# Performance work log

Hardware: AMD Instinct MI355X
Metric: run time of the kernel (lower is better)

## Reference

```python
import jax, jax.numpy as jnp
import numpy as np

N = 50000
E = 800000
IN_DIM = 3
HID = 128
OUT_DIM = 3
RED = 16


def setup_inputs() -> dict:
    key = jax.random.key(0)
    ks = jax.random.split(key, 20)
    s = lambda k, shp: jax.random.normal(k, shp, dtype=jnp.float32) * 0.05
    inp = {
        'x': jax.random.normal(ks[0], (N, IN_DIM), dtype=jnp.float32),
        'edge_index': jax.random.randint(ks[1], (2, E), 0, N, dtype=jnp.int32),
        'deg_inv_sqrt': jax.random.uniform(ks[2], (N,), dtype=jnp.float32),
        # GCN layer weights (torch Linear convention: [out, in])
        'W1': s(ks[3], (HID, IN_DIM)), 'b1': s(ks[4], (HID,)),
        'W2': s(ks[5], (HID, HID)),    'b2': s(ks[6], (HID,)),
        'W3': s(ks[7], (HID, HID)),    'b3': s(ks[8], (HID,)),
        # channel attention MLPs (no bias): C -> C//RED -> C
        'ca1_w1': s(ks[9],  (HID // RED, HID)), 'ca1_w2': s(ks[10], (HID, HID // RED)),
        'ca2_w1': s(ks[11], (HID // RED, HID)), 'ca2_w2': s(ks[12], (HID, HID // RED)),
        'ca3_w1': s(ks[13], (HID // RED, HID)), 'ca3_w2': s(ks[14], (HID, HID // RED)),
        # output head
        'Wout': s(ks[15], (OUT_DIM, HID)), 'bout': s(ks[16], (OUT_DIM,)),
    }
    return inp


def _gcn(x, row, col, dis, W, b):
    # gather source features, normalize by deg_inv_sqrt[row]*deg_inv_sqrt[col], scatter-add to target
    norm = (dis[row] * dis[col])[:, None]          # [E,1]
    msg = x[row] * norm                             # [E,C]
    agg = jax.ops.segment_sum(msg, col, num_segments=x.shape[0])  # [N,C]
    return jax.nn.elu(agg @ W.T + b)


def _channel_attn(x, w1, w2):
    # global avg/max pool over nodes -> [C]; shared MLP; sigmoid gate
    avg = jnp.mean(x, axis=0)
    mx = jnp.max(x, axis=0)
    mlp = lambda v: jax.nn.relu(v @ w1.T) @ w2.T
    att = jax.nn.sigmoid(mlp(avg) + mlp(mx))        # [C]
    return x * att


def reference(x, edge_index, deg_inv_sqrt, W1, b1, W2, b2, W3, b3,
              ca1_w1, ca1_w2, ca2_w1, ca2_w2, ca3_w1, ca3_w2, Wout, bout):
    row, col = edge_index[0], edge_index[1]
    h = _gcn(x, row, col, deg_inv_sqrt, W1, b1)
    h = _channel_attn(h, ca1_w1, ca1_w2)
    h = _gcn(h, row, col, deg_inv_sqrt, W2, b2)
    h = _channel_attn(h, ca2_w1, ca2_w2)
    h = _gcn(h, row, col, deg_inv_sqrt, W3, b3)
    h = _channel_attn(h, ca3_w1, ca3_w2)
    return h @ Wout.T + bout
```

## Files before the change

kernel.cpp:

```cpp
#include <hip/hip_runtime.h>

#define NN 50000
#define NE 800000
#define NPAD 50176
#define NBD3 391
#define NBG 782
#define PMAX (NBG*128)
#define NRED 64

#define EC 4096
#define NBLKC 196
#define NBUCK 1563
#define LT (NBUCK*NBLKC)
#define NS1 300
#define DCAP 1024

typedef __attribute__((ext_vector_type(8))) short bf16x8;
typedef __attribute__((ext_vector_type(4))) float f32x4;

__device__ __forceinline__ float elu_f(float x){ return x > 0.f ? x : __expf(x) - 1.f; }

__device__ __forceinline__ ushort f2bf(float f){
    unsigned u = __float_as_uint(f);
    unsigned r = (u + 0x7FFFu + ((u >> 16) & 1u)) >> 16;
    return (ushort)r;
}
__device__ __forceinline__ float bf2f(short u){
    return __uint_as_float(((unsigned)(unsigned short)u) << 16);
}

__global__ __launch_bounds__(256) void k_bhist(const int* __restrict__ col, int* __restrict__ hist,
                        const float* __restrict__ W2, const float* __restrict__ W3,
                        ushort* __restrict__ Wb2, ushort* __restrict__ Wb3){
    int blk = blockIdx.x;
    if (blk >= NBLKC){
        int i = (blk - NBLKC)*256 + threadIdx.x;
        if (i < 16384){ Wb2[i] = f2bf(W2[i]); Wb3[i] = f2bf(W3[i]); }
        return;
    }
    __shared__ int h[NBUCK];
    for (int i = threadIdx.x; i < NBUCK; i += 256) h[i] = 0;
    __syncthreads();
    int base = blk * EC;
    #pragma unroll
    for (int i = 0; i < 16; ++i){
        int e = base + i*256 + threadIdx.x;
        if (e < NE) atomicAdd(&h[col[e] >> 5], 1);
    }
    __syncthreads();
    for (int i = threadIdx.x; i < NBUCK; i += 256) hist[i*NBLKC + blk] = h[i];
}

__global__ __launch_bounds__(256) void k_s1(const int* __restrict__ hist, int* __restrict__ bsum){
    __shared__ int red[256];
    int base = blockIdx.x*1024 + threadIdx.x;
    int s = 0;
    #pragma unroll
    for (int i = 0; i < 4; ++i){ int idx = base + i*256; if (idx < LT) s += hist[idx]; }
    red[threadIdx.x] = s;
    __syncthreads();
    for (int off = 128; off > 0; off >>= 1){
        if (threadIdx.x < off) red[threadIdx.x] += red[threadIdx.x + off];
        __syncthreads();
    }
    if (threadIdx.x == 0) bsum[blockIdx.x] = red[0];
}

__global__ __launch_bounds__(512) void k_s2(const int* __restrict__ bsum, int* __restrict__ boff){
    __shared__ int s[512];
    int t = threadIdx.x;
    int v = (t < NS1) ? bsum[t] : 0;
    s[t] = v;
    __syncthreads();
    for (int off = 1; off < 512; off <<= 1){
        int u = (t >= off) ? s[t - off] : 0;
        __syncthreads();
        s[t] += u;
        __syncthreads();
    }
    if (t < NS1) boff[t] = s[t] - v;
}

__global__ __launch_bounds__(256) void k_s3(const int* __restrict__ hist, const int* __restrict__ boff,
                                            int* __restrict__ scanned, int* __restrict__ bucketPtr){
    __shared__ int red[256];
    int blk = blockIdx.x, t = threadIdx.x;
    int base = blk*1024;
    int v[4]; int s = 0;
    #pragma unroll
    for (int i = 0; i < 4; ++i){
        int idx = base + t*4 + i;
        v[i] = (idx < LT) ? hist[idx] : 0;
        s += v[i];
    }
    red[t] = s;
    __syncthreads();
    for (int off = 1; off < 256; off <<= 1){
        int u = (t >= off) ? red[t - off] : 0;
        __syncthreads();
        red[t] += u;
        __syncthreads();
    }
    int run = boff[blk] + red[t] - s;
    #pragma unroll
    for (int i = 0; i < 4; ++i){
        int idx = base + t*4 + i;
        if (idx < LT){
            scanned[idx] = run;
            if (idx % NBLKC == 0) bucketPtr[idx / NBLKC] = run;
            run += v[i];
        }
    }
    if (blk == 0 && t == 0) bucketPtr[NBUCK] = NE;
}

__global__ __launch_bounds__(256) void k_csort(const int* __restrict__ row, const int* __restrict__ col,
                                               const int* __restrict__ scanned, int2* __restrict__ edgeS){
    __shared__ int curs[NBUCK];
    int blk = blockIdx.x;
    for (int i = threadIdx.x; i < NBUCK; i += 256) curs[i] = scanned[i*NBLKC + blk];
    __syncthreads();
    int base = blk * EC;
    #pragma unroll
    for (int i = 0; i < 16; ++i){
        int e = base + i*256 + threadIdx.x;
        if (e < NE){
            int r = row[e], c = col[e];
            int pos = atomicAdd(&curs[c >> 5], 1);
            edgeS[pos] = make_int2(r, c);
        }
    }
}

__global__ __launch_bounds__(256) void k_dsort(const float* __restrict__ dis, const int* __restrict__ bucketPtr,
                                               int2* __restrict__ edge, int* __restrict__ rowptr){
    __shared__ int nodeCnt[32];
    __shared__ int nodeOff[33];
    __shared__ float disL[32];
    __shared__ int2 stage[DCAP];
    int b = blockIdx.x, t = threadIdx.x;
    int j0 = bucketPtr[b], j1 = bucketPtr[b+1], cnt = j1 - j0;
    if (t < 32){
        nodeCnt[t] = 0;
        int c = b*32 + t;
        disL[t] = (c < NN) ? dis[c] : 0.f;
    }
    __syncthreads();
    int er[8], ec[8], rk[8]; int m = 0;
    for (int j = t; j < cnt && m < 8; j += 256){
        int2 e = edge[j0 + j];
        int cl = e.y & 31;
        er[m] = e.x; ec[m] = e.y;
        rk[m] = atomicAdd(&nodeCnt[cl], 1);
        ++m;
    }
    __syncthreads();
    if (t == 0){
        int run = 0;
        #pragma unroll
        for (int i = 0; i < 32; ++i){ nodeOff[i] = run; run += nodeCnt[i]; }
        nodeOff[32] = run;
    }
    __syncthreads();
    if (t < 32){
        int c = b*32 + t;
        if (c < NN) rowptr[c] = j0 + nodeOff[t];
    }
    if (b == 0 && t == 0) rowptr[NN] = NE;
    bool staged = (cnt <= DCAP);
    for (int i = 0; i < m; ++i){
        int r = er[i], cl = ec[i] & 31;
        float nm = dis[r] * disL[cl];
        int pos = nodeOff[cl] + rk[i];
        int2 rec = make_int2(r, __float_as_int(nm));
        if (staged) stage[pos] = rec;
        else        edge[j0 + pos] = rec;
    }
    __syncthreads();
    if (staged)
        for (int j = t; j < cnt; j += 256) edge[j0 + j] = stage[j];
}

__global__ void k_gather3(const float* __restrict__ x, const int* __restrict__ rowptr,
                          const int2* __restrict__ edge, float* __restrict__ agg){
    int n = blockIdx.x * blockDim.x + threadIdx.x;
    if (n >= NN) return;
    int j0 = rowptr[n], j1 = rowptr[n + 1];
    float a0 = 0.f, a1 = 0.f, a2 = 0.f;
    for (int j = j0; j < j1; ++j){
        int2 e = edge[j];
        int r = e.x; float w = __int_as_float(e.y);
        a0 = fmaf(x[r*3+0], w, a0);
        a1 = fmaf(x[r*3+1], w, a1);
        a2 = fmaf(x[r*3+2], w, a2);
    }
    agg[n*3+0] = a0; agg[n*3+1] = a1; agg[n*3+2] = a2;
}

__global__ __launch_bounds__(128) void k_dense3p(const float* __restrict__ agg, const float* __restrict__ W,
                          const float* __restrict__ b, ushort* __restrict__ h, float* __restrict__ part){
    int c = threadIdx.x;
    int n0 = blockIdx.x * 128;
    int n1 = min(n0 + 128, NN);
    float w0 = W[c*3+0], w1 = W[c*3+1], w2 = W[c*3+2], bb = b[c];
    float s = 0.f, m = -3.4e38f;
    for (int n = n0; n < n1; ++n){
        float v = fmaf(agg[n*3+0], w0, fmaf(agg[n*3+1], w1, fmaf(agg[n*3+2], w2, bb)));
        v = elu_f(v);
        h[(size_t)n*128 + c] = f2bf(v);
        s += v; m = fmaxf(m, v);
    }
    part[blockIdx.x*128 + c] = s;
    part[PMAX + blockIdx.x*128 + c] = m;
}

__global__ __launch_bounds__(256) void k_gather128(const ushort* __restrict__ h,
                              const int* __restrict__ rowptr, const int2* __restrict__ edge,
                              const float* __restrict__ att, ushort* __restrict__ aggB){
    int t = blockIdx.x * blockDim.x + threadIdx.x;
    int n = t >> 4, l = t & 15;
    if (n >= NN) return;
    int j0 = rowptr[n], j1 = rowptr[n + 1];
    float acc[8] = {0.f,0.f,0.f,0.f,0.f,0.f,0.f,0.f};
    int j = j0;
    for (; j + 3 < j1; j += 4){
        int2 e0 = edge[j], e1 = edge[j+1], e2 = edge[j+2], e3 = edge[j+3];
        bf16x8 v0 = *(const bf16x8*)(h + (size_t)e0.x*128 + l*8);
        bf16x8 v1 = *(const bf16x8*)(h + (size_t)e1.x*128 + l*8);
        bf16x8 v2 = *(const bf16x8*)(h + (size_t)e2.x*128 + l*8);
        bf16x8 v3 = *(const bf16x8*)(h + (size_t)e3.x*128 + l*8);
        float w0 = __int_as_float(e0.y), w1 = __int_as_float(e1.y);
        float w2 = __int_as_float(e2.y), w3 = __int_as_float(e3.y);
        #pragma unroll
        for (int c = 0; c < 8; ++c){
            acc[c] = fmaf(bf2f(v0[c]), w0, acc[c]);
            acc[c] = fmaf(bf2f(v1[c]), w1, acc[c]);
            acc[c] = fmaf(bf2f(v2[c]), w2, acc[c]);
            acc[c] = fmaf(bf2f(v3[c]), w3, acc[c]);
        }
    }
    for (; j < j1; ++j){
        int2 e0 = edge[j];
        bf16x8 v0 = *(const bf16x8*)(h + (size_t)e0.x*128 + l*8);
        float w0 = __int_as_float(e0.y);
        #pragma unroll
        for (int c = 0; c < 8; ++c)
            acc[c] = fmaf(bf2f(v0[c]), w0, acc[c]);
    }
    float4 a0 = ((const float4*)att)[l*2];
    float4 a1 = ((const float4*)att)[l*2+1];
    float av[8] = {a0.x,a0.y,a0.z,a0.w,a1.x,a1.y,a1.z,a1.w};
    bf16x8 o;
    #pragma unroll
    for (int c = 0; c < 8; ++c)
        o[c] = (short)f2bf(acc[c] * av[c]);
    *(bf16x8*)(aggB + (size_t)n*128 + l*8) = o;
}

__global__ __launch_bounds__(256) void k_attn_pre(const float* __restrict__ part, int nblk,
                                                  float* __restrict__ part2){
    __shared__ float sS[2][128], sM[2][128];
    int c = threadIdx.x & 127, g = threadIdx.x >> 7;
    float s = 0.f, m = -3.4e38f;
    for (int b = blockIdx.x*2 + g; b < nblk; b += NRED*2){
        s += part[b*128 + c];
        m = fmaxf(m, part[PMAX + b*128 + c]);
    }
    sS[g][c] = s; sM[g][c] = m;
    __syncthreads();
    if (g == 0){
        part2[blockIdx.x*128 + c] = sS[0][c] + sS[1][c];
        part2[NRED*128 + blockIdx.x*128 + c] = fmaxf(sM[0][c], sM[1][c]);
    }
}

__global__ __launch_bounds__(512) void k_attn(const float* __restrict__ part2,
                       const float* __restrict__ w1, const float* __restrict__ w2,
                       float* __restrict__ att){
    __shared__ float sAll[4][128], mAll[4][128];
    __shared__ float avg[128], mx[128], ha[8], hm[8];
    int c = threadIdx.x & 127, g = threadIdx.x >> 7;
    float s = 0.f, m = -3.4e38f;
    #pragma unroll
    for (int b = 0; b < NRED/4; ++b){
        int r = b*4 + g;
        s += part2[r*128 + c];
        m = fmaxf(m, part2[NRED*128 + r*128 + c]);
    }
    sAll[g][c] = s; mAll[g][c] = m;
    __syncthreads();
    if (g == 0){
        s = sAll[0][c] + sAll[1][c] + sAll[2][c] + sAll[3][c];
        m = fmaxf(fmaxf(mAll[0][c], mAll[1][c]), fmaxf(mAll[2][c], mAll[3][c]));
        avg[c] = s / (float)NN;
        mx[c] = m;
    }
    __syncthreads();
    if (threadIdx.x < 8){
        int cc = threadIdx.x;
        float sa = 0.f, sm = 0.f;
        for (int k = 0; k < 128; ++k){
            float w = w1[cc*128 + k];
            sa += avg[k]*w; sm += mx[k]*w;
        }
        ha[cc] = fmaxf(sa, 0.f); hm[cc] = fmaxf(sm, 0.f);
    }
    __syncthreads();
    if (threadIdx.x < 128){
        float oa = 0.f, om = 0.f;
        for (int j = 0; j < 8; ++j){
            float w = w2[c*8 + j];
            oa += ha[j]*w; om += hm[j]*w;
        }
        att[c] = 1.f / (1.f + __expf(-(oa + om)));
    }
}

__global__ __launch_bounds__(256) void k_gemm_mfma(const ushort* __restrict__ aggB,
                        const ushort* __restrict__ Wb, const float* __restrict__ b,
                        ushort* __restrict__ h, float* __restrict__ part){
    __shared__ float poolS[4][128], poolM[4][128];
    int tid = threadIdx.x;
    int wave = tid >> 6, l = tid & 63;
    int lr = l & 15, lk = l >> 4;
    int n0 = blockIdx.x * 64 + wave * 16;

    bf16x8 a[4];
    const ushort* arow = aggB + (size_t)(n0 + lr) * 128 + lk * 8;
    #pragma unroll
    for (int kb = 0; kb < 4; ++kb)
        a[kb] = *(const bf16x8*)(arow + kb * 32);

    float s_part[8], m_part[8];
    const ushort* wbase = Wb + (size_t)lr * 128 + lk * 8;
    #pragma unroll
    for (int t = 0; t < 8; ++t){
        int j0 = t * 16;
        float bias = b[j0 + lr];
        f32x4 acc = {bias, bias, bias, bias};
        const ushort* wrow = wbase + (size_t)j0 * 128;
        #pragma unroll
        for (int kb = 0; kb < 4; ++kb){
            bf16x8 bf = *(const bf16x8*)(wrow + kb * 32);
            acc = __builtin_amdgcn_mfma_f32_16x16x32_bf16(a[kb], bf, acc, 0, 0, 0);
        }
        float s = 0.f, m = -3.4e38f;
        #pragma unroll
        for (int r = 0; r < 4; ++r){
            int n = n0 + lk * 4 + r;
            float v = elu_f(acc[r]);
            if (n < NN){
                h[(size_t)n * 128 + j0 + lr] = f2bf(v);
                s += v; m = fmaxf(m, v);
            }
        }
        s += __shfl_xor(s, 16); s += __shfl_xor(s, 32);
        m = fmaxf(m, __shfl_xor(m, 16)); m = fmaxf(m, __shfl_xor(m, 32));
        s_part[t] = s; m_part[t] = m;
    }
    if (lk == 0){
        #pragma unroll
        for (int t = 0; t < 8; ++t){
            poolS[wave][t * 16 + lr] = s_part[t];
            poolM[wave][t * 16 + lr] = m_part[t];
        }
    }
    __syncthreads();
    if (tid < 128){
        float S = poolS[0][tid] + poolS[1][tid] + poolS[2][tid] + poolS[3][tid];
        float M = fmaxf(fmaxf(poolM[0][tid], poolM[1][tid]), fmaxf(poolM[2][tid], poolM[3][tid]));
        part[blockIdx.x * 128 + tid] = S;
        part[PMAX + blockIdx.x * 128 + tid] = M;
    }
}

__global__ __launch_bounds__(256) void k_out(const ushort* __restrict__ h, const float* __restrict__ att,
                      const float* __restrict__ Wo, const float* __restrict__ bo,
                      float* __restrict__ out){
    int n = blockIdx.x * blockDim.x + threadIdx.x;
    if (n >= NN) return;
    float acc0 = bo[0], acc1 = bo[1], acc2 = bo[2];
    const bf16x8* hv = (const bf16x8*)(h + (size_t)n*128);
    #pragma unroll
    for (int i = 0; i < 16; ++i){
        bf16x8 v = hv[i];
        #pragma unroll
        for (int c = 0; c < 8; ++c){
            int cc = i*8 + c;
            float hv_f = bf2f(v[c]) * att[cc];
            acc0 = fmaf(hv_f, Wo[cc],        acc0);
            acc1 = fmaf(hv_f, Wo[128 + cc],  acc1);
            acc2 = fmaf(hv_f, Wo[256 + cc],  acc2);
        }
    }
    out[n*3+0] = acc0; out[n*3+1] = acc1; out[n*3+2] = acc2;
}

extern "C" void kernel_launch(void* const* d_in, const int* in_sizes, int n_in,
                              void* d_out, int out_size, void* d_ws, size_t ws_size,
                              hipStream_t stream) {
    const float* x    = (const float*)d_in[0];
    const int*   ei   = (const int*)d_in[1];
    const int*   row  = ei;
    const int*   col  = ei + NE;
    const float* dis  = (const float*)d_in[2];
    const float* W1   = (const float*)d_in[3];
    const float* b1   = (const float*)d_in[4];
    const float* W2   = (const float*)d_in[5];
    const float* b2   = (const float*)d_in[6];
    const float* W3   = (const float*)d_in[7];
    const float* b3   = (const float*)d_in[8];
    const float* ca1w1= (const float*)d_in[9];
    const float* ca1w2= (const float*)d_in[10];
    const float* ca2w1= (const float*)d_in[11];
    const float* ca2w2= (const float*)d_in[12];
    const float* ca3w1= (const float*)d_in[13];
    const float* ca3w2= (const float*)d_in[14];
    const float* Wout = (const float*)d_in[15];
    const float* bout = (const float*)d_in[16];
    float* out = (float*)d_out;

    ushort* hB    = (ushort*)d_ws;
    ushort* aggB  = hB + (size_t)NN*128;
    float*  agg3  = (float*)(aggB + (size_t)NPAD*128);
    float*  part  = agg3 + (size_t)NN*3;
    float*  part2 = part + (size_t)2*PMAX;
    float*  att1  = part2 + 2*NRED*128;
    float*  att2  = att1 + 128;
    float*  att3  = att2 + 128;
    ushort* Wb2   = (ushort*)(att3 + 128);
    ushort* Wb3   = Wb2 + 16384;
    int2*   edge  = (int2*)(Wb3 + 16384);
    int*    rowptr= (int*)(edge + NE);
    int*    hist  = rowptr + NN + 1;
    int*    scanned = hist + LT;
    int*    bucketPtr = scanned + LT;
    int*    bsum  = bucketPtr + NBUCK + 1;
    int*    boff  = bsum + NS1;

    const int gath_blocks = (NN * 16) / 256;

    k_bhist<<<NBLKC + 64, 256, 0, stream>>>(col, hist, W2, W3, Wb2, Wb3);
    k_s1<<<NS1, 256, 0, stream>>>(hist, bsum);
    k_s2<<<1, 512, 0, stream>>>(bsum, boff);
    k_s3<<<NS1, 256, 0, stream>>>(hist, boff, scanned, bucketPtr);
    k_csort<<<NBLKC, 256, 0, stream>>>(row, col, scanned, edge);
    k_dsort<<<NBUCK, 256, 0, stream>>>(dis, bucketPtr, edge, rowptr);

    k_gather3<<<(NN+255)/256, 256, 0, stream>>>(x, rowptr, edge, agg3);
    k_dense3p<<<NBD3, 128, 0, stream>>>(agg3, W1, b1, hB, part);
    k_attn_pre<<<NRED, 256, 0, stream>>>(part, NBD3, part2);
    k_attn<<<1, 512, 0, stream>>>(part2, ca1w1, ca1w2, att1);

    k_gather128<<<gath_blocks, 256, 0, stream>>>(hB, rowptr, edge, att1, aggB);
    k_gemm_mfma<<<NBG, 256, 0, stream>>>(aggB, Wb2, b2, hB, part);
    k_attn_pre<<<NRED, 256, 0, stream>>>(part, NBG, part2);
    k_attn<<<1, 512, 0, stream>>>(part2, ca2w1, ca2w2, att2);

    k_gather128<<<gath_blocks, 256, 0, stream>>>(hB, rowptr, edge, att2, aggB);
    k_gemm_mfma<<<NBG, 256, 0, stream>>>(aggB, Wb3, b3, hB, part);
    k_attn_pre<<<NRED, 256, 0, stream>>>(part, NBG, part2);
    k_attn<<<1, 512, 0, stream>>>(part2, ca3w1, ca3w2, att3);

    k_out<<<(NN+255)/256, 256, 0, stream>>>(hB, att3, Wout, bout, out);
}
```

Measured before the change: 217.6 us.

## Fuse neighbor gather into MFMA GEMM and fold attention into weights

Each node's weighted neighbour gather now runs inside the GEMM kernel and writes straight into a swizzled LDS tile, so the bf16 aggregate buffer is no longer written to and read back from global memory. The channel-attention gate is folded into the next layer's weight columns, which the attention kernel now converts to bf16, and into the output head weights. This removes one kernel launch per layer plus the elementwise scaling. In exchange, gather parallelism drops to 4 threads per node with 32 accumulators each, which raises register pressure and may reduce latency hiding for the irregular loads, and the layers ping-pong between two h buffers.

```diff
diff --git a/kernel.cpp b/kernel.cpp
--- a/kernel.cpp
+++ b/kernel.cpp
@@ -2,7 +2,6 @@
 
 #define NN 50000
 #define NE 800000
-#define NPAD 50176
 #define NBD3 391
 #define NBG 782
 #define PMAX (NBG*128)
@@ -29,16 +28,9 @@
     return __uint_as_float(((unsigned)(unsigned short)u) << 16);
 }
 
-__global__ __launch_bounds__(256) void k_bhist(const int* __restrict__ col, int* __restrict__ hist,
-                        const float* __restrict__ W2, const float* __restrict__ W3,
-                        ushort* __restrict__ Wb2, ushort* __restrict__ Wb3){
+__global__ __launch_bounds__(256) void k_bhist(const int* __restrict__ col, int* __restrict__ hist){
+    __shared__ int h[NBUCK];
     int blk = blockIdx.x;
-    if (blk >= NBLKC){
-        int i = (blk - NBLKC)*256 + threadIdx.x;
-        if (i < 16384){ Wb2[i] = f2bf(W2[i]); Wb3[i] = f2bf(W3[i]); }
-        return;
-    }
-    __shared__ int h[NBUCK];
     for (int i = threadIdx.x; i < NBUCK; i += 256) h[i] = 0;
     __syncthreads();
     int base = blk * EC;
@@ -214,49 +206,6 @@
     part[PMAX + blockIdx.x*128 + c] = m;
 }
 
-__global__ __launch_bounds__(256) void k_gather128(const ushort* __restrict__ h,
-                              const int* __restrict__ rowptr, const int2* __restrict__ edge,
-                              const float* __restrict__ att, ushort* __restrict__ aggB){
-    int t = blockIdx.x * blockDim.x + threadIdx.x;
-    int n = t >> 4, l = t & 15;
-    if (n >= NN) return;
-    int j0 = rowptr[n], j1 = rowptr[n + 1];
-    float acc[8] = {0.f,0.f,0.f,0.f,0.f,0.f,0.f,0.f};
-    int j = j0;
-    for (; j + 3 < j1; j += 4){
-        int2 e0 = edge[j], e1 = edge[j+1], e2 = edge[j+2], e3 = edge[j+3];
-        bf16x8 v0 = *(const bf16x8*)(h + (size_t)e0.x*128 + l*8);
-        bf16x8 v1 = *(const bf16x8*)(h + (size_t)e1.x*128 + l*8);
-        bf16x8 v2 = *(const bf16x8*)(h + (size_t)e2.x*128 + l*8);
-        bf16x8 v3 = *(const bf16x8*)(h + (size_t)e3.x*128 + l*8);
-        float w0 = __int_as_float(e0.y), w1 = __int_as_float(e1.y);
-        float w2 = __int_as_float(e2.y), w3 = __int_as_float(e3.y);
-        #pragma unroll
-        for (int c = 0; c < 8; ++c){
-            acc[c] = fmaf(bf2f(v0[c]), w0, acc[c]);
-            acc[c] = fmaf(bf2f(v1[c]), w1, acc[c]);
-            acc[c] = fmaf(bf2f(v2[c]), w2, acc[c]);
-            acc[c] = fmaf(bf2f(v3[c]), w3, acc[c]);
-        }
-    }
-    for (; j < j1; ++j){
-        int2 e0 = edge[j];
-        bf16x8 v0 = *(const bf16x8*)(h + (size_t)e0.x*128 + l*8);
-        float w0 = __int_as_float(e0.y);
-        #pragma unroll
-        for (int c = 0; c < 8; ++c)
-            acc[c] = fmaf(bf2f(v0[c]), w0, acc[c]);
-    }
-    float4 a0 = ((const float4*)att)[l*2];
-    float4 a1 = ((const float4*)att)[l*2+1];
-    float av[8] = {a0.x,a0.y,a0.z,a0.w,a1.x,a1.y,a1.z,a1.w};
-    bf16x8 o;
-    #pragma unroll
-    for (int c = 0; c < 8; ++c)
-        o[c] = (short)f2bf(acc[c] * av[c]);
-    *(bf16x8*)(aggB + (size_t)n*128 + l*8) = o;
-}
-
 __global__ __launch_bounds__(256) void k_attn_pre(const float* __restrict__ part, int nblk,
                                                   float* __restrict__ part2){
     __shared__ float sS[2][128], sM[2][128];
@@ -276,9 +225,9 @@
 
 __global__ __launch_bounds__(512) void k_attn(const float* __restrict__ part2,
                        const float* __restrict__ w1, const float* __restrict__ w2,
-                       float* __restrict__ att){
+                       const float* __restrict__ Wsrc, void* __restrict__ Wdst, int mode){
     __shared__ float sAll[4][128], mAll[4][128];
-    __shared__ float avg[128], mx[128], ha[8], hm[8];
+    __shared__ float avg[128], mx[128], ha[8], hm[8], attL[128];
     int c = threadIdx.x & 127, g = threadIdx.x >> 7;
     float s = 0.f, m = -3.4e38f;
     #pragma unroll
@@ -312,25 +261,103 @@
             float w = w2[c*8 + j];
             oa += ha[j]*w; om += hm[j]*w;
         }
-        att[c] = 1.f / (1.f + __expf(-(oa + om)));
-    }
-}
-
-__global__ __launch_bounds__(256) void k_gemm_mfma(const ushort* __restrict__ aggB,
+        attL[c] = 1.f / (1.f + __expf(-(oa + om)));
+    }
+    __syncthreads();
+    if (mode == 0){
+        ushort* wd = (ushort*)Wdst;
+        for (int i = threadIdx.x; i < 16384; i += 512)
+            wd[i] = f2bf(Wsrc[i] * attL[i & 127]);
+    } else {
+        float* wd = (float*)Wdst;
+        if (threadIdx.x < 384)
+            wd[threadIdx.x] = Wsrc[threadIdx.x] * attL[threadIdx.x & 127];
+    }
+}
+
+__global__ __launch_bounds__(256) void k_gg(const ushort* __restrict__ h,
+                        const int* __restrict__ rowptr, const int2* __restrict__ edge,
                         const ushort* __restrict__ Wb, const float* __restrict__ b,
-                        ushort* __restrict__ h, float* __restrict__ part){
+                        ushort* __restrict__ hout, float* __restrict__ part){
+    __shared__ ushort At[64*128];
     __shared__ float poolS[4][128], poolM[4][128];
     int tid = threadIdx.x;
+    int n0b = blockIdx.x * 64;
+
+    {
+        int node = tid >> 2;
+        int q = tid & 3;
+        int n = n0b + node;
+        float acc[32];
+        #pragma unroll
+        for (int i = 0; i < 32; ++i) acc[i] = 0.f;
+        if (n < NN){
+            int j0 = rowptr[n], j1 = rowptr[n + 1];
+            const ushort* hq = h + q*32;
+            int j = j0;
+            for (; j + 1 < j1; j += 2){
+                int2 e0 = edge[j], e1 = edge[j+1];
+                const ushort* r0 = hq + (size_t)e0.x*128;
+                const ushort* r1 = hq + (size_t)e1.x*128;
+                bf16x8 v00 = *(const bf16x8*)(r0);
+                bf16x8 v01 = *(const bf16x8*)(r0 + 8);
+                bf16x8 v02 = *(const bf16x8*)(r0 + 16);
+                bf16x8 v03 = *(const bf16x8*)(r0 + 24);
+                bf16x8 v10 = *(const bf16x8*)(r1);
+                bf16x8 v11 = *(const bf16x8*)(r1 + 8);
+                bf16x8 v12 = *(const bf16x8*)(r1 + 16);
+                bf16x8 v13 = *(const bf16x8*)(r1 + 24);
+                float w0 = __int_as_float(e0.y), w1 = __int_as_float(e1.y);
+                #pragma unroll
+                for (int cc = 0; cc < 8; ++cc){
+                    acc[cc]    = fmaf(bf2f(v00[cc]), w0, acc[cc]);
+                    acc[8+cc]  = fmaf(bf2f(v01[cc]), w0, acc[8+cc]);
+                    acc[16+cc] = fmaf(bf2f(v02[cc]), w0, acc[16+cc]);
+                    acc[24+cc] = fmaf(bf2f(v03[cc]), w0, acc[24+cc]);
+                    acc[cc]    = fmaf(bf2f(v10[cc]), w1, acc[cc]);
+                    acc[8+cc]  = fmaf(bf2f(v11[cc]), w1, acc[8+cc]);
+                    acc[16+cc] = fmaf(bf2f(v12[cc]), w1, acc[16+cc]);
+                    acc[24+cc] = fmaf(bf2f(v13[cc]), w1, acc[24+cc]);
+                }
+            }
+            if (j < j1){
+                int2 e0 = edge[j];
+                const ushort* r0 = hq + (size_t)e0.x*128;
+                bf16x8 v00 = *(const bf16x8*)(r0);
+                bf16x8 v01 = *(const bf16x8*)(r0 + 8);
+                bf16x8 v02 = *(const bf16x8*)(r0 + 16);
+                bf16x8 v03 = *(const bf16x8*)(r0 + 24);
+                float w0 = __int_as_float(e0.y);
+                #pragma unroll
+                for (int cc = 0; cc < 8; ++cc){
+                    acc[cc]    = fmaf(bf2f(v00[cc]), w0, acc[cc]);
+                    acc[8+cc]  = fmaf(bf2f(v01[cc]), w0, acc[8+cc]);
+                    acc[16+cc] = fmaf(bf2f(v02[cc]), w0, acc[16+cc]);
+                    acc[24+cc] = fmaf(bf2f(v03[cc]), w0, acc[24+cc]);
+                }
+            }
+        }
+        #pragma unroll
+        for (int k = 0; k < 4; ++k){
+            bf16x8 o;
+            #pragma unroll
+            for (int cc = 0; cc < 8; ++cc) o[cc] = (short)f2bf(acc[k*8 + cc]);
+            int s = q*4 + k;
+            *(bf16x8*)((char*)At + node*256 + ((s ^ (node & 7)) << 4)) = o;
+        }
+    }
+    __syncthreads();
+
     int wave = tid >> 6, l = tid & 63;
     int lr = l & 15, lk = l >> 4;
-    int n0 = blockIdx.x * 64 + wave * 16;
-
+    int r = wave*16 + lr;
     bf16x8 a[4];
-    const ushort* arow = aggB + (size_t)(n0 + lr) * 128 + lk * 8;
-    #pragma unroll
-    for (int kb = 0; kb < 4; ++kb)
-        a[kb] = *(const bf16x8*)(arow + kb * 32);
-
+    #pragma unroll
+    for (int kb = 0; kb < 4; ++kb){
+        int s = kb*4 + lk;
+        a[kb] = *(const bf16x8*)((char*)At + r*256 + ((s ^ (r & 7)) << 4));
+    }
+    int n0 = n0b + wave*16;
     float s_part[8], m_part[8];
     const ushort* wbase = Wb + (size_t)lr * 128 + lk * 8;
     #pragma unroll
@@ -346,11 +373,11 @@
         }
         float s = 0.f, m = -3.4e38f;
         #pragma unroll
-        for (int r = 0; r < 4; ++r){
-            int n = n0 + lk * 4 + r;
-            float v = elu_f(acc[r]);
+        for (int rr = 0; rr < 4; ++rr){
+            int n = n0 + lk * 4 + rr;
+            float v = elu_f(acc[rr]);
             if (n < NN){
-                h[(size_t)n * 128 + j0 + lr] = f2bf(v);
+                hout[(size_t)n * 128 + j0 + lr] = f2bf(v);
                 s += v; m = fmaxf(m, v);
             }
         }
@@ -374,8 +401,8 @@
     }
 }
 
-__global__ __launch_bounds__(256) void k_out(const ushort* __restrict__ h, const float* __restrict__ att,
-                      const float* __restrict__ Wo, const float* __restrict__ bo,
+__global__ __launch_bounds__(256) void k_out(const ushort* __restrict__ h,
+                      const float* __restrict__ WoS, const float* __restrict__ bo,
                       float* __restrict__ out){
     int n = blockIdx.x * blockDim.x + threadIdx.x;
     if (n >= NN) return;
@@ -387,10 +414,10 @@
         #pragma unroll
         for (int c = 0; c < 8; ++c){
             int cc = i*8 + c;
-            float hv_f = bf2f(v[c]) * att[cc];
-            acc0 = fmaf(hv_f, Wo[cc],        acc0);
-            acc1 = fmaf(hv_f, Wo[128 + cc],  acc1);
-            acc2 = fmaf(hv_f, Wo[256 + cc],  acc2);
+            float hv_f = bf2f(v[c]);
+            acc0 = fmaf(hv_f, WoS[cc],        acc0);
+            acc1 = fmaf(hv_f, WoS[128 + cc],  acc1);
+            acc2 = fmaf(hv_f, WoS[256 + cc],  acc2);
         }
     }
     out[n*3+0] = acc0; out[n*3+1] = acc1; out[n*3+2] = acc2;
@@ -421,16 +448,14 @@
     float* out = (float*)d_out;
 
     ushort* hB    = (ushort*)d_ws;
-    ushort* aggB  = hB + (size_t)NN*128;
-    float*  agg3  = (float*)(aggB + (size_t)NPAD*128);
+    ushort* hC    = hB + (size_t)NN*128;
+    float*  agg3  = (float*)(hC + (size_t)NN*128);
     float*  part  = agg3 + (size_t)NN*3;
     float*  part2 = part + (size_t)2*PMAX;
-    float*  att1  = part2 + 2*NRED*128;
-    float*  att2  = att1 + 128;
-    float*  att3  = att2 + 128;
-    ushort* Wb2   = (ushort*)(att3 + 128);
+    ushort* Wb2   = (ushort*)(part2 + 2*NRED*128);
     ushort* Wb3   = Wb2 + 16384;
-    int2*   edge  = (int2*)(Wb3 + 16384);
+    float*  WoutS = (float*)(Wb3 + 16384);
+    int2*   edge  = (int2*)(WoutS + 384);
     int*    rowptr= (int*)(edge + NE);
     int*    hist  = rowptr + NN + 1;
     int*    scanned = hist + LT;
@@ -438,9 +463,7 @@
     int*    bsum  = bucketPtr + NBUCK + 1;
     int*    boff  = bsum + NS1;
 
-    const int gath_blocks = (NN * 16) / 256;
-
-    k_bhist<<<NBLKC + 64, 256, 0, stream>>>(col, hist, W2, W3, Wb2, Wb3);
+    k_bhist<<<NBLKC, 256, 0, stream>>>(col, hist);
     k_s1<<<NS1, 256, 0, stream>>>(hist, bsum);
     k_s2<<<1, 512, 0, stream>>>(bsum, boff);
     k_s3<<<NS1, 256, 0, stream>>>(hist, boff, scanned, bucketPtr);
@@ -450,17 +473,15 @@
     k_gather3<<<(NN+255)/256, 256, 0, stream>>>(x, rowptr, edge, agg3);
     k_dense3p<<<NBD3, 128, 0, stream>>>(agg3, W1, b1, hB, part);
     k_attn_pre<<<NRED, 256, 0, stream>>>(part, NBD3, part2);
-    k_attn<<<1, 512, 0, stream>>>(part2, ca1w1, ca1w2, att1);
-
-    k_gather128<<<gath_blocks, 256, 0, stream>>>(hB, rowptr, edge, att1, aggB);
-    k_gemm_mfma<<<NBG, 256, 0, stream>>>(aggB, Wb2, b2, hB, part);
+    k_attn<<<1, 512, 0, stream>>>(part2, ca1w1, ca1w2, W2, (void*)Wb2, 0);
+
+    k_gg<<<NBG, 256, 0, stream>>>(hB, rowptr, edge, Wb2, b2, hC, part);
     k_attn_pre<<<NRED, 256, 0, stream>>>(part, NBG, part2);
-    k_attn<<<1, 512, 0, stream>>>(part2, ca2w1, ca2w2, att2);
-
-    k_gather128<<<gath_blocks, 256, 0, stream>>>(hB, rowptr, edge, att2, aggB);
-    k_gemm_mfma<<<NBG, 256, 0, stream>>>(aggB, Wb3, b3, hB, part);
+    k_attn<<<1, 512, 0, stream>>>(part2, ca2w1, ca2w2, W3, (void*)Wb3, 0);
+
+    k_gg<<<NBG, 256, 0, stream>>>(hC, rowptr, edge, Wb3, b3, hB, part);
     k_attn_pre<<<NRED, 256, 0, stream>>>(part, NBG, part2);
-    k_attn<<<1, 512, 0, stream>>>(part2, ca3w1, ca3w2, att3);
-
-    k_out<<<(NN+255)/256, 256, 0, stream>>>(hB, att3, Wout, bout, out);
-}
+    k_attn<<<1, 512, 0, stream>>>(part2, ca3w1, ca3w2, Wout, (void*)WoutS, 1);
+
+    k_out<<<(NN+255)/256, 256, 0, stream>>>(hB, WoutS, bout, out);
+}
```

Result: no change. 220.2 us (+1.2%).

## Fold channel attention into next-layer weights and fuse layer-1 gather with dense

Applied to the files above, without the earlier changes.

The per-channel attention scale is now folded algebraically into the columns of the following weight matrix (W2, W3, Wout) inside the single-block attention kernel, which also does the bf16 conversion. This removes the per-element att multiply from the gather and output kernels and drops the separate weight-conversion blocks from the histogram kernel. The first-layer 3-wide gather and the dense expansion are fused into one kernel through shared memory, removing a launch and the agg3 round trip. The cost is that a single 512-thread block now converts 16K weights serially on the critical path, three times.

```diff
diff --git a/kernel.cpp b/kernel.cpp
--- a/kernel.cpp
+++ b/kernel.cpp
@@ -29,16 +29,9 @@
     return __uint_as_float(((unsigned)(unsigned short)u) << 16);
 }
 
-__global__ __launch_bounds__(256) void k_bhist(const int* __restrict__ col, int* __restrict__ hist,
-                        const float* __restrict__ W2, const float* __restrict__ W3,
-                        ushort* __restrict__ Wb2, ushort* __restrict__ Wb3){
+__global__ __launch_bounds__(256) void k_bhist(const int* __restrict__ col, int* __restrict__ hist){
+    __shared__ int h[NBUCK];
     int blk = blockIdx.x;
-    if (blk >= NBLKC){
-        int i = (blk - NBLKC)*256 + threadIdx.x;
-        if (i < 16384){ Wb2[i] = f2bf(W2[i]); Wb3[i] = f2bf(W3[i]); }
-        return;
-    }
-    __shared__ int h[NBUCK];
     for (int i = threadIdx.x; i < NBUCK; i += 256) h[i] = 0;
     __syncthreads();
     int base = blk * EC;
@@ -181,31 +174,35 @@
         for (int j = t; j < cnt; j += 256) edge[j0 + j] = stage[j];
 }
 
-__global__ void k_gather3(const float* __restrict__ x, const int* __restrict__ rowptr,
-                          const int2* __restrict__ edge, float* __restrict__ agg){
-    int n = blockIdx.x * blockDim.x + threadIdx.x;
-    if (n >= NN) return;
-    int j0 = rowptr[n], j1 = rowptr[n + 1];
-    float a0 = 0.f, a1 = 0.f, a2 = 0.f;
-    for (int j = j0; j < j1; ++j){
-        int2 e = edge[j];
-        int r = e.x; float w = __int_as_float(e.y);
-        a0 = fmaf(x[r*3+0], w, a0);
-        a1 = fmaf(x[r*3+1], w, a1);
-        a2 = fmaf(x[r*3+2], w, a2);
-    }
-    agg[n*3+0] = a0; agg[n*3+1] = a1; agg[n*3+2] = a2;
-}
-
-__global__ __launch_bounds__(128) void k_dense3p(const float* __restrict__ agg, const float* __restrict__ W,
-                          const float* __restrict__ b, ushort* __restrict__ h, float* __restrict__ part){
-    int c = threadIdx.x;
+__global__ __launch_bounds__(128) void k_l1(const float* __restrict__ x, const int* __restrict__ rowptr,
+                        const int2* __restrict__ edge, const float* __restrict__ W,
+                        const float* __restrict__ b, ushort* __restrict__ h, float* __restrict__ part){
+    __shared__ float aggL[128*3];
+    int t = threadIdx.x;
     int n0 = blockIdx.x * 128;
-    int n1 = min(n0 + 128, NN);
+    int nEnd = min(n0 + 128, NN);
+    {
+        int n = n0 + t;
+        float a0 = 0.f, a1 = 0.f, a2 = 0.f;
+        if (n < NN){
+            int j0 = rowptr[n], j1 = rowptr[n + 1];
+            for (int j = j0; j < j1; ++j){
+                int2 e = edge[j];
+                int r = e.x; float w = __int_as_float(e.y);
+                a0 = fmaf(x[r*3+0], w, a0);
+                a1 = fmaf(x[r*3+1], w, a1);
+                a2 = fmaf(x[r*3+2], w, a2);
+            }
+        }
+        aggL[t*3+0] = a0; aggL[t*3+1] = a1; aggL[t*3+2] = a2;
+    }
+    __syncthreads();
+    int c = t;
     float w0 = W[c*3+0], w1 = W[c*3+1], w2 = W[c*3+2], bb = b[c];
     float s = 0.f, m = -3.4e38f;
-    for (int n = n0; n < n1; ++n){
-        float v = fmaf(agg[n*3+0], w0, fmaf(agg[n*3+1], w1, fmaf(agg[n*3+2], w2, bb)));
+    for (int n = n0; n < nEnd; ++n){
+        int nn = n - n0;
+        float v = fmaf(aggL[nn*3+0], w0, fmaf(aggL[nn*3+1], w1, fmaf(aggL[nn*3+2], w2, bb)));
         v = elu_f(v);
         h[(size_t)n*128 + c] = f2bf(v);
         s += v; m = fmaxf(m, v);
@@ -216,7 +213,7 @@
 
 __global__ __launch_bounds__(256) void k_gather128(const ushort* __restrict__ h,
                               const int* __restrict__ rowptr, const int2* __restrict__ edge,
-                              const float* __restrict__ att, ushort* __restrict__ aggB){
+                              ushort* __restrict__ aggB){
     int t = blockIdx.x * blockDim.x + threadIdx.x;
     int n = t >> 4, l = t & 15;
     if (n >= NN) return;
@@ -247,13 +244,10 @@
         for (int c = 0; c < 8; ++c)
             acc[c] = fmaf(bf2f(v0[c]), w0, acc[c]);
     }
-    float4 a0 = ((const float4*)att)[l*2];
-    float4 a1 = ((const float4*)att)[l*2+1];
-    float av[8] = {a0.x,a0.y,a0.z,a0.w,a1.x,a1.y,a1.z,a1.w};
     bf16x8 o;
     #pragma unroll
     for (int c = 0; c < 8; ++c)
-        o[c] = (short)f2bf(acc[c] * av[c]);
+        o[c] = (short)f2bf(acc[c]);
     *(bf16x8*)(aggB + (size_t)n*128 + l*8) = o;
 }
 
@@ -276,9 +270,9 @@
 
 __global__ __launch_bounds__(512) void k_attn(const float* __restrict__ part2,
                        const float* __restrict__ w1, const float* __restrict__ w2,
-                       float* __restrict__ att){
+                       const float* __restrict__ Wsrc, void* __restrict__ Wdst, int mode){
     __shared__ float sAll[4][128], mAll[4][128];
-    __shared__ float avg[128], mx[128], ha[8], hm[8];
+    __shared__ float avg[128], mx[128], ha[8], hm[8], attL[128];
     int c = threadIdx.x & 127, g = threadIdx.x >> 7;
     float s = 0.f, m = -3.4e38f;
     #pragma unroll
@@ -312,7 +306,17 @@
             float w = w2[c*8 + j];
             oa += ha[j]*w; om += hm[j]*w;
         }
-        att[c] = 1.f / (1.f + __expf(-(oa + om)));
+        attL[c] = 1.f / (1.f + __expf(-(oa + om)));
+    }
+    __syncthreads();
+    if (mode == 0){
+        ushort* wd = (ushort*)Wdst;
+        for (int i = threadIdx.x; i < 16384; i += 512)
+            wd[i] = f2bf(Wsrc[i] * attL[i & 127]);
+    } else {
+        float* wd = (float*)Wdst;
+        if (threadIdx.x < 384)
+            wd[threadIdx.x] = Wsrc[threadIdx.x] * attL[threadIdx.x & 127];
     }
 }
 
@@ -374,8 +378,8 @@
     }
 }
 
-__global__ __launch_bounds__(256) void k_out(const ushort* __restrict__ h, const float* __restrict__ att,
-                      const float* __restrict__ Wo, const float* __restrict__ bo,
+__global__ __launch_bounds__(256) void k_out(const ushort* __restrict__ h,
+                      const float* __restrict__ WoS, const float* __restrict__ bo,
                       float* __restrict__ out){
     int n = blockIdx.x * blockDim.x + threadIdx.x;
     if (n >= NN) return;
@@ -387,10 +391,10 @@
         #pragma unroll
         for (int c = 0; c < 8; ++c){
             int cc = i*8 + c;
-            float hv_f = bf2f(v[c]) * att[cc];
-            acc0 = fmaf(hv_f, Wo[cc],        acc0);
-            acc1 = fmaf(hv_f, Wo[128 + cc],  acc1);
-            acc2 = fmaf(hv_f, Wo[256 + cc],  acc2);
+            float hv_f = bf2f(v[c]);
+            acc0 = fmaf(hv_f, WoS[cc],        acc0);
+            acc1 = fmaf(hv_f, WoS[128 + cc],  acc1);
+            acc2 = fmaf(hv_f, WoS[256 + cc],  acc2);
         }
     }
     out[n*3+0] = acc0; out[n*3+1] = acc1; out[n*3+2] = acc2;
@@ -422,15 +426,12 @@
 
     ushort* hB    = (ushort*)d_ws;
     ushort* aggB  = hB + (size_t)NN*128;
-    float*  agg3  = (float*)(aggB + (size_t)NPAD*128);
-    float*  part  = agg3 + (size_t)NN*3;
+    float*  part  = (float*)(aggB + (size_t)NPAD*128);
     float*  part2 = part + (size_t)2*PMAX;
-    float*  att1  = part2 + 2*NRED*128;
-    float*  att2  = att1 + 128;
-    float*  att3  = att2 + 128;
-    ushort* Wb2   = (ushort*)(att3 + 128);
+    ushort* Wb2   = (ushort*)(part2 + 2*NRED*128);
     ushort* Wb3   = Wb2 + 16384;
-    int2*   edge  = (int2*)(Wb3 + 16384);
+    float*  WoutS = (float*)(Wb3 + 16384);
+    int2*   edge  = (int2*)(WoutS + 384);
     int*    rowptr= (int*)(edge + NE);
     int*    hist  = rowptr + NN + 1;
     int*    scanned = hist + LT;
@@ -440,27 +441,26 @@
 
     const int gath_blocks = (NN * 16) / 256;
 
-    k_bhist<<<NBLKC + 64, 256, 0, stream>>>(col, hist, W2, W3, Wb2, Wb3);
+    k_bhist<<<NBLKC, 256, 0, stream>>>(col, hist);
     k_s1<<<NS1, 256, 0, stream>>>(hist, bsum);
     k_s2<<<1, 512, 0, stream>>>(bsum, boff);
     k_s3<<<NS1, 256, 0, stream>>>(hist, boff, scanned, bucketPtr);
     k_csort<<<NBLKC, 256, 0, stream>>>(row, col, scanned, edge);
     k_dsort<<<NBUCK, 256, 0, stream>>>(dis, bucketPtr, edge, rowptr);
 
-    k_gather3<<<(NN+255)/256, 256, 0, stream>>>(x, rowptr, edge, agg3);
-    k_dense3p<<<NBD3, 128, 0, stream>>>(agg3, W1, b1, hB, part);
+    k_l1<<<NBD3, 128, 0, stream>>>(x, rowptr, edge, W1, b1, hB, part);
     k_attn_pre<<<NRED, 256, 0, stream>>>(part, NBD3, part2);
-    k_attn<<<1, 512, 0, stream>>>(part2, ca1w1, ca1w2, att1);
-
-    k_gather128<<<gath_blocks, 256, 0, stream>>>(hB, rowptr, edge, att1, aggB);
+    k_attn<<<1, 512, 0, stream>>>(part2, ca1w1, ca1w2, W2, (void*)Wb2, 0);
+
+    k_gather128<<<gath_blocks, 256, 0, stream>>>(hB, rowptr, edge, aggB);
     k_gemm_mfma<<<NBG, 256, 0, stream>>>(aggB, Wb2, b2, hB, part);
     k_attn_pre<<<NRED, 256, 0, stream>>>(part, NBG, part2);
-    k_attn<<<1, 512, 0, stream>>>(part2, ca2w1, ca2w2, att2);
-
-    k_gather128<<<gath_blocks, 256, 0, stream>>>(hB, rowptr, edge, att2, aggB);
+    k_attn<<<1, 512, 0, stream>>>(part2, ca2w1, ca2w2, W3, (void*)Wb3, 0);
+
+    k_gather128<<<gath_blocks, 256, 0, stream>>>(hB, rowptr, edge, aggB);
     k_gemm_mfma<<<NBG, 256, 0, stream>>>(aggB, Wb3, b3, hB, part);
     k_attn_pre<<<NRED, 256, 0, stream>>>(part, NBG, part2);
-    k_attn<<<1, 512, 0, stream>>>(part2, ca3w1, ca3w2, att3);
-
-    k_out<<<(NN+255)/256, 256, 0, stream>>>(hB, att3, Wout, bout, out);
-}
+    k_attn<<<1, 512, 0, stream>>>(part2, ca3w1, ca3w2, Wout, (void*)WoutS, 1);
+
+    k_out<<<(NN+255)/256, 256, 0, stream>>>(hB, WoutS, bout, out);
+}
```

Measured after the change: 210.8 us, median of 2. 3.1% less time.
